# Kernel optimization log

Hardware: AMD Instinct MI355X
Metric: run time of the kernel (lower is better)

## Reference

```python
import jax, jax.numpy as jnp
import numpy as np

B, S, H = 2, 2048, 2048
NH, NKV, D = 32, 8, 64
N_REP = NH // NKV  # 4
THETA = 10000.0


def _rotate_half(x):
    x1, x2 = jnp.split(x, 2, axis=-1)
    return jnp.concatenate([-x2, x1], axis=-1)


def _apply_rope(q, k, position_ids):
    # q: [B,NH,S,D], k: [B,NKV,S,D], position_ids: [B,S]
    inv_freq = 1.0 / (THETA ** (jnp.arange(0, D, 2, dtype=jnp.float32) / D))  # [D/2]
    ang = position_ids[:, None, :, None].astype(jnp.float32) * inv_freq      # [B,1,S,D/2]
    cos = jnp.concatenate([jnp.cos(ang), jnp.cos(ang)], axis=-1)             # [B,1,S,D]
    sin = jnp.concatenate([jnp.sin(ang), jnp.sin(ang)], axis=-1)
    q = q * cos + _rotate_half(q) * sin
    k = k * cos + _rotate_half(k) * sin
    return q, k


def setup_inputs() -> dict:
    key = jax.random.key(0)
    k1, k2, k3, k4 = jax.random.split(key, 4)
    hidden_states = jax.random.normal(k1, (B, S, H), dtype=jnp.float32)
    position_ids = jnp.broadcast_to(jnp.arange(S, dtype=jnp.int64 if jax.config.jax_enable_x64 else jnp.int32)[None, :], (B, S))
    Wq = jax.random.normal(k2, (H, NH * D), dtype=jnp.float32) * 0.02
    Wkv = jax.random.normal(k3, (H, NKV * 2 * D), dtype=jnp.float32) * 0.02
    Wo = jax.random.normal(k4, (H, H), dtype=jnp.float32) * 0.02
    return {"hidden_states": hidden_states, "position_ids": position_ids,
            "Wq": Wq, "Wkv": Wkv, "Wo": Wo}


def reference(hidden_states, position_ids, Wq, Wkv, Wo):
    b, s, _ = hidden_states.shape
    # fused QKV projections (Linear, no bias)
    q = (hidden_states @ Wq).reshape(b, s, NH, D).transpose(0, 2, 1, 3)      # [B,NH,S,D]
    kv = (hidden_states @ Wkv).reshape(b, s, NKV, 2, D)
    k = kv[:, :, :, 0, :].transpose(0, 2, 1, 3)                              # [B,NKV,S,D]
    v = kv[:, :, :, 1, :].transpose(0, 2, 1, 3)                              # [B,NKV,S,D]
    # rotary embedding
    q, k = _apply_rope(q, k, position_ids)
    # GQA: repeat_interleave K/V heads
    k = jnp.repeat(k, N_REP, axis=1)                                         # [B,NH,S,D]
    v = jnp.repeat(v, N_REP, axis=1)
    # causal SDPA (eval mode: dropout_p = 0)
    scale = 1.0 / np.sqrt(D)
    scores = jnp.einsum('bhqd,bhkd->bhqk', q, k) * scale                     # [B,NH,S,S]
    causal = jnp.tril(jnp.ones((s, s), dtype=bool))
    scores = jnp.where(causal[None, None], scores, jnp.finfo(scores.dtype).min)
    probs = jax.nn.softmax(scores, axis=-1)
    ctx = jnp.einsum('bhqk,bhkd->bhqd', probs, v)                            # [B,NH,S,D]
    ctx = ctx.transpose(0, 2, 1, 3).reshape(b, s, H)
    return ctx @ Wo
```

## Files before the change

kernel.cpp:

```cpp
#include <hip/hip_runtime.h>

typedef __bf16 bf16_t;
typedef __bf16 bf16x8 __attribute__((ext_vector_type(8)));
typedef __bf16 bf16x4 __attribute__((ext_vector_type(4)));
typedef float f32x4 __attribute__((ext_vector_type(4)));

#define DEV static __device__ __forceinline__

DEV void gload16(const void* g, void* lds) {
  __builtin_amdgcn_global_load_lds((__attribute__((address_space(1))) void*)g,
                                   (__attribute__((address_space(3))) void*)lds, 16, 0, 0);
}

DEV f32x4 mfma16(bf16x8 a, bf16x8 b, f32x4 c) {
  return __builtin_amdgcn_mfma_f32_16x16x32_bf16(a, b, c, 0, 0, 0);
}

DEV void transpose_blk(const float* __restrict__ in, bf16_t* __restrict__ out,
                       int R, int C, int bx, int by, int tid, float (*tile)[33]) {
  const int tx = tid & 31, ty = tid >> 5;
  const int rb = by * 32, cb = bx * 32;
#pragma unroll
  for (int i = 0; i < 32; i += 8)
    tile[ty + i][tx] = in[(size_t)(rb + ty + i) * C + (cb + tx)];
  __syncthreads();
#pragma unroll
  for (int i = 0; i < 32; i += 8)
    out[(size_t)(cb + ty + i) * R + (rb + tx)] = (bf16_t)tile[tx][ty + i];
}

__global__ __launch_bounds__(256) void k_prep(const float* __restrict__ hs,
                                              bf16_t* __restrict__ Xbf,
                                              const float* __restrict__ Wq,
                                              const float* __restrict__ Wkv,
                                              const float* __restrict__ Wo,
                                              bf16_t* __restrict__ Wqkvt,
                                              bf16_t* __restrict__ Wot,
                                              const int* __restrict__ pos_ids,
                                              float2* __restrict__ tbl) {
  __shared__ float tile[32][33];
  const int bid = blockIdx.x, tid = threadIdx.x;
  if (bid < 8192) {
    const int i = (bid * 256 + tid) * 4;
    float4 v = *(const float4*)(hs + i);
    bf16x4 o;
    o[0] = (bf16_t)v.x; o[1] = (bf16_t)v.y; o[2] = (bf16_t)v.z; o[3] = (bf16_t)v.w;
    *(bf16x4*)(Xbf + i) = o;
  } else if (bid < 8192 + 512) {
    const int token = (bid - 8192) * 8 + (tid >> 5);
    const int d2 = tid & 31;
    const float p = (float)pos_ids[token];
    const float freq = exp2f(-(float)d2 / 32.0f * log2f(10000.0f));
    const float a = p * freq;
    tbl[token * 32 + d2] = make_float2(cosf(a), sinf(a));
  } else if (bid < 8192 + 512 + 4096) {
    const int local = bid - (8192 + 512);
    transpose_blk(Wq, Wqkvt, 2048, 2048, local & 63, local >> 6, tid, tile);
  } else if (bid < 8192 + 512 + 4096 + 2048) {
    const int local = bid - (8192 + 512 + 4096);
    transpose_blk(Wkv, Wqkvt + (size_t)2048 * 2048, 2048, 1024,
                  local & 31, local >> 5, tid, tile);
  } else {
    const int local = bid - (8192 + 512 + 4096 + 2048);
    transpose_blk(Wo, Wot, 2048, 2048, local & 63, local >> 6, tid, tile);
  }
}

#define PH_MID()                                            \
  __builtin_amdgcn_s_barrier();                             \
  asm volatile("s_waitcnt lgkmcnt(0)" ::: "memory");        \
  __builtin_amdgcn_sched_barrier(0);                        \
  __builtin_amdgcn_s_setprio(1)

#define PH_END()                                            \
  __builtin_amdgcn_s_setprio(0);                            \
  __builtin_amdgcn_s_barrier()

#define STAGE_A(bi, st, h)                                                      \
  do {                                                                          \
    const bf16_t* _s = gA + (size_t)(brow + (h) * 128 + r0) * gK + (st) * 64 + l0 * 8; \
    gload16(_s, &As[bi][((h) * 1024 + tid) * 8]);                               \
    gload16(_s + (size_t)64 * gK, &As[bi][((h) * 1024 + 512 + tid) * 8]);       \
  } while (0)

#define STAGE_B(bi, st, h)                                                      \
  do {                                                                          \
    const bf16_t* _s = gB + (size_t)(bcol + (h) * 128 + r0) * gK + (st) * 64 + l0 * 8; \
    gload16(_s, &Bs[bi][((h) * 1024 + tid) * 8]);                               \
    gload16(_s + (size_t)64 * gK, &Bs[bi][((h) * 1024 + 512 + tid) * 8]);       \
  } while (0)

#define LOADA(bi, mh)                                                           \
  _Pragma("unroll")                                                             \
  for (int mq = 0; mq < 4; ++mq) {                                              \
    const int R = wm * 128 + (mh) * 64 + mq * 16 + c15;                         \
    af[mq][0] = *(const bf16x8*)(&As[bi][(R * 8 + (g ^ (R & 7))) * 8]);         \
    af[mq][1] = *(const bf16x8*)(&As[bi][(R * 8 + ((4 + g) ^ (R & 7))) * 8]);   \
  }

#define LOADB(bi, nh)                                                           \
  _Pragma("unroll")                                                             \
  for (int nq = 0; nq < 2; ++nq) {                                              \
    const int R = wn * 64 + ((nh) * 2 + nq) * 16 + c15;                         \
    bfr[nq][0] = *(const bf16x8*)(&Bs[bi][(R * 8 + (g ^ (R & 7))) * 8]);        \
    bfr[nq][1] = *(const bf16x8*)(&Bs[bi][(R * 8 + ((4 + g) ^ (R & 7))) * 8]);  \
  }

#define MFMAQ(mh, nh)                                                           \
  _Pragma("unroll")                                                             \
  for (int nq = 0; nq < 2; ++nq)                                                \
    _Pragma("unroll")                                                           \
    for (int mq = 0; mq < 4; ++mq)                                              \
      acc[(mh) * 4 + mq][(nh) * 2 + nq] =                                       \
          mfma16(af[mq][1], bfr[nq][1],                                         \
                 mfma16(af[mq][0], bfr[nq][0], acc[(mh) * 4 + mq][(nh) * 2 + nq]));

__global__ __launch_bounds__(512, 2) void k_gemm_qkv(
    const bf16_t* __restrict__ gA, const bf16_t* __restrict__ gB,
    const float2* __restrict__ tbl,
    bf16_t* __restrict__ Qp, bf16_t* __restrict__ Kp, bf16_t* __restrict__ Vt) {
  __shared__ __align__(16) bf16_t As[2][256 * 64];
  __shared__ __align__(16) bf16_t Bs[2][256 * 64];
  const int gK = 2048, NBX = 12;
  const int tid = threadIdx.x;
  const int lane = tid & 63, w = tid >> 6;
  const int c15 = lane & 15, g = lane >> 4;
  const int wm = w >> 2, wn = w & 3;

  const int cpx = (int)gridDim.x >> 3;
  const int u = ((int)blockIdx.x & 7) * cpx + ((int)blockIdx.x >> 3);
  const int bx = u % NBX, by = u / NBX;
  const int brow = by * 256, bcol = bx * 256;

  const int r0 = tid >> 3, p0 = tid & 7;
  const int l0 = p0 ^ (r0 & 7);

  const f32x4 fzero = {0.f, 0.f, 0.f, 0.f};
  f32x4 acc[8][4];
#pragma unroll
  for (int m = 0; m < 8; ++m)
#pragma unroll
    for (int n = 0; n < 4; ++n) acc[m][n] = fzero;

  const int NT = gK >> 6;

  STAGE_A(0, 0, 0); STAGE_A(0, 0, 1); STAGE_B(0, 0, 0); STAGE_B(0, 0, 1);
  STAGE_A(1, 1, 0);
  asm volatile("s_waitcnt vmcnt(2)" ::: "memory");
  __builtin_amdgcn_s_barrier();

  for (int t = 0; t < NT; ++t) {
    const int bi = t & 1, oi = bi ^ 1;
    const int st1 = (t + 1 < NT) ? t + 1 : NT - 1;
    const int st2 = (t + 2 < NT) ? t + 2 : NT - 1;
    bf16x8 af[4][2], bfr[2][2];

    LOADA(bi, 0);
    LOADB(bi, 0);
    STAGE_A(oi, st1, 1);
    STAGE_B(oi, st1, 0);
    PH_MID();
    MFMAQ(0, 0);
    PH_END();

    LOADB(bi, 1);
    STAGE_B(oi, st1, 1);
    PH_MID();
    MFMAQ(0, 1);
    PH_END();

    LOADA(bi, 1);
    LOADB(bi, 0);
    PH_MID();
    MFMAQ(1, 0);
    PH_END();

    LOADB(bi, 1);
    STAGE_A(bi, st2, 0);
    asm volatile("s_waitcnt vmcnt(2)" ::: "memory");
    PH_MID();
    MFMAQ(1, 1);
    PH_END();
  }

  const int seg = bcol + wn * 64;
  const int wrow = brow + wm * 128;
  const float QSCALE = 0.125f * 1.44269504088896340736f;
  if (seg < 2048) {
    const int hq = seg >> 6;
#pragma unroll
    for (int m = 0; m < 8; ++m)
#pragma unroll
      for (int r = 0; r < 4; ++r) {
        const int row = wrow + m * 16 + g * 4 + r;
        const int bb = row >> 11, s = row & 2047;
        const float2 cs0 = tbl[row * 32 + c15];
        const float2 cs1 = tbl[row * 32 + 16 + c15];
        bf16_t* dst = Qp + (((size_t)bb * 32 + hq) * 2048 + s) * 64;
        dst[c15]      = (bf16_t)((acc[m][0][r] * cs0.x - acc[m][2][r] * cs0.y) * QSCALE);
        dst[32 + c15] = (bf16_t)((acc[m][2][r] * cs0.x + acc[m][0][r] * cs0.y) * QSCALE);
        dst[16 + c15] = (bf16_t)((acc[m][1][r] * cs1.x - acc[m][3][r] * cs1.y) * QSCALE);
        dst[48 + c15] = (bf16_t)((acc[m][3][r] * cs1.x + acc[m][1][r] * cs1.y) * QSCALE);
      }
  } else {
    const int cc = seg - 2048;
    const int kvh = cc >> 7;
    if (((cc >> 6) & 1) == 0) {
#pragma unroll
      for (int m = 0; m < 8; ++m)
#pragma unroll
        for (int r = 0; r < 4; ++r) {
          const int row = wrow + m * 16 + g * 4 + r;
          const int bb = row >> 11, s = row & 2047;
          const float2 cs0 = tbl[row * 32 + c15];
          const float2 cs1 = tbl[row * 32 + 16 + c15];
          bf16_t* dst = Kp + (((size_t)bb * 8 + kvh) * 2048 + s) * 64;
          dst[c15]      = (bf16_t)(acc[m][0][r] * cs0.x - acc[m][2][r] * cs0.y);
          dst[32 + c15] = (bf16_t)(acc[m][2][r] * cs0.x + acc[m][0][r] * cs0.y);
          dst[16 + c15] = (bf16_t)(acc[m][1][r] * cs1.x - acc[m][3][r] * cs1.y);
          dst[48 + c15] = (bf16_t)(acc[m][3][r] * cs1.x + acc[m][1][r] * cs1.y);
        }
    } else {
#pragma unroll
      for (int m = 0; m < 8; ++m) {
        const int row0 = wrow + m * 16 + g * 4;
        const int bb = row0 >> 11, s0 = row0 & 2047;
#pragma unroll
        for (int n = 0; n < 4; ++n) {
          bf16x4 o;
#pragma unroll
          for (int r = 0; r < 4; ++r) o[r] = (bf16_t)acc[m][n][r];
          const int d = n * 16 + c15;
          *(bf16x4*)(Vt + ((size_t)(bb * 8 + kvh) * 64 + d) * 2048 + s0) = o;
        }
      }
    }
  }
}

#define OSTAGE_A(bi, st, h)                                                     \
  do {                                                                          \
    const bf16_t* _s = gA + (size_t)(brow + (h) * 128 + r0) * gK + (st) * 64 + l0 * 8; \
    gload16(_s, &As[bi][((h) * 1024 + tid) * 8]);                               \
    gload16(_s + (size_t)64 * gK, &As[bi][((h) * 1024 + 512 + tid) * 8]);       \
  } while (0)

#define OSTAGE_B(bi, st)                                                        \
  do {                                                                          \
    const bf16_t* _s = gB + (size_t)(bcol + r0) * gK + (st) * 64 + l0 * 8;      \
    gload16(_s, &Bs[bi][tid * 8]);                                              \
    gload16(_s + (size_t)64 * gK, &Bs[bi][(512 + tid) * 8]);                    \
  } while (0)

#define OLOADB(bi)                                                              \
  _Pragma("unroll")                                                             \
  for (int nq = 0; nq < 2; ++nq) {                                              \
    const int R = wn * 32 + nq * 16 + c15;                                      \
    bfr[nq][0] = *(const bf16x8*)(&Bs[bi][(R * 8 + (g ^ (R & 7))) * 8]);        \
    bfr[nq][1] = *(const bf16x8*)(&Bs[bi][(R * 8 + ((4 + g) ^ (R & 7))) * 8]);  \
  }

#define OMFMAQ(mh)                                                              \
  _Pragma("unroll")                                                             \
  for (int nq = 0; nq < 2; ++nq)                                                \
    _Pragma("unroll")                                                           \
    for (int mq = 0; mq < 4; ++mq)                                              \
      acc[(mh) * 4 + mq][nq] =                                                  \
          mfma16(af[mq][1], bfr[nq][1],                                         \
                 mfma16(af[mq][0], bfr[nq][0], acc[(mh) * 4 + mq][nq]));

__global__ __launch_bounds__(512, 2) void k_gemm_out(
    const bf16_t* __restrict__ gA, const bf16_t* __restrict__ gB,
    float* __restrict__ C) {
  __shared__ __align__(16) bf16_t As[2][256 * 64];
  __shared__ __align__(16) bf16_t Bs[2][128 * 64];
  const int gK = 2048, NBX = 16, ldc = 2048;
  const int tid = threadIdx.x;
  const int lane = tid & 63, w = tid >> 6;
  const int c15 = lane & 15, g = lane >> 4;
  const int wm = w >> 2, wn = w & 3;

  const int cpx = (int)gridDim.x >> 3;
  const int u = ((int)blockIdx.x & 7) * cpx + ((int)blockIdx.x >> 3);
  const int bx = u % NBX, by = u / NBX;
  const int brow = by * 256, bcol = bx * 128;

  const int r0 = tid >> 3, p0 = tid & 7;
  const int l0 = p0 ^ (r0 & 7);

  const f32x4 fzero = {0.f, 0.f, 0.f, 0.f};
  f32x4 acc[8][2];
#pragma unroll
  for (int m = 0; m < 8; ++m)
#pragma unroll
    for (int n = 0; n < 2; ++n) acc[m][n] = fzero;

  const int NT = gK >> 6;

  OSTAGE_A(0, 0, 0); OSTAGE_A(0, 0, 1); OSTAGE_B(0, 0);
  OSTAGE_A(1, 1, 0); OSTAGE_B(1, 1);
  asm volatile("s_waitcnt vmcnt(4)" ::: "memory");
  __builtin_amdgcn_s_barrier();

  for (int t = 0; t < NT; ++t) {
    const int bi = t & 1, oi = bi ^ 1;
    const int st1 = (t + 1 < NT) ? t + 1 : NT - 1;
    const int st2 = (t + 2 < NT) ? t + 2 : NT - 1;
    bf16x8 af[4][2], bfr[2][2];

    LOADA(bi, 0);
    OLOADB(bi);
    OSTAGE_A(oi, st1, 1);
    PH_MID();
    OMFMAQ(0);
    PH_END();

    LOADA(bi, 1);
    OSTAGE_A(bi, st2, 0);
    OSTAGE_B(bi, st2);
    asm volatile("s_waitcnt vmcnt(4)" ::: "memory");
    PH_MID();
    OMFMAQ(1);
    PH_END();
  }

#pragma unroll
  for (int m = 0; m < 8; ++m)
#pragma unroll
    for (int n = 0; n < 2; ++n)
#pragma unroll
      for (int r = 0; r < 4; ++r) {
        const int row = brow + wm * 128 + m * 16 + g * 4 + r;
        const int col = bcol + wn * 32 + n * 16 + c15;
        C[(size_t)row * ldc + col] = acc[m][n][r];
      }
}

__global__ __launch_bounds__(256, 3) void k_attn(const bf16_t* __restrict__ Qp,
                                                 const bf16_t* __restrict__ Kp,
                                                 const bf16_t* __restrict__ Vt,
                                                 bf16_t* __restrict__ ctx) {
  const int wgid = blockIdx.x;
  const int gidx = wgid & 15;
  const int j    = wgid >> 4;
  const int b = gidx >> 3, kvh = gidx & 7;
  const int qs = 63 - j;
  const int tid = threadIdx.x, lane = tid & 63, w = tid >> 6;
  const int h = kvh * 4 + w;
  const int c15 = lane & 15, g = lane >> 4;

  __shared__ __align__(16) bf16_t Ks[2][64 * 64];
  __shared__ __align__(16) bf16_t Vs[2][64 * 64];
  __shared__ __align__(16) bf16_t Pw[4][32 * 64];
  bf16_t* pw = &Pw[w][0];

  const int q0 = qs * 32;

  bf16x8 aq[2][2];
#pragma unroll
  for (int m = 0; m < 2; ++m) {
    const bf16_t* Qrow = Qp + (((size_t)b * 32 + h) * 2048 + q0 + m * 16 + c15) * 64;
    aq[m][0] = *(const bf16x8*)(Qrow + g * 8);
    aq[m][1] = *(const bf16x8*)(Qrow + 32 + g * 8);
  }
  asm volatile("s_waitcnt vmcnt(0)" ::: "memory");

  const bf16_t* Kb = Kp + ((size_t)b * 8 + kvh) * (size_t)(2048 * 64);
  const bf16_t* Vb = Vt + ((size_t)b * 8 + kvh) * (size_t)(64 * 2048);

  const int c0 = tid,      r0 = c0 >> 3, l0 = (c0 & 7) ^ (r0 & 7);
  const int c1 = tid + 256, r1 = c1 >> 3, l1 = (c1 & 7) ^ (r1 & 7);
  const int dst0 = (w * 64) * 8, dst1 = (w * 64 + 256) * 8;

  const f32x4 fzero = {0.f, 0.f, 0.f, 0.f};
  f32x4 acc[2][4];
  f32x4 lsum[2];
#pragma unroll
  for (int m = 0; m < 2; ++m) {
    lsum[m] = fzero;
#pragma unroll
    for (int n = 0; n < 4; ++n) acc[m][n] = fzero;
  }
  bf16x8 bones;
#pragma unroll
  for (int j2 = 0; j2 < 8; ++j2) bones[j2] = (bf16_t)1.0f;

  const int ntw = qs / 2 + 1;

  gload16(Kb + (size_t)r0 * 64 + l0 * 8, &Ks[0][dst0]);
  gload16(Kb + (size_t)r1 * 64 + l1 * 8, &Ks[0][dst1]);
  gload16(Vb + (size_t)r0 * 2048 + l0 * 8, &Vs[0][dst0]);
  gload16(Vb + (size_t)r1 * 2048 + l1 * 8, &Vs[0][dst1]);

  for (int t = 0; t < ntw; ++t) {
    const int kvbase = t * 64;
    const int tnb = (t + 1 < ntw ? t + 1 : t) * 64;
    const int nb = (t + 1) & 1, cb = t & 1;

    gload16(Kb + (size_t)(tnb + r0) * 64 + l0 * 8, &Ks[nb][dst0]);
    gload16(Kb + (size_t)(tnb + r1) * 64 + l1 * 8, &Ks[nb][dst1]);
    gload16(Vb + (size_t)r0 * 2048 + tnb + l0 * 8, &Vs[nb][dst0]);
    gload16(Vb + (size_t)r1 * 2048 + tnb + l1 * 8, &Vs[nb][dst1]);
    asm volatile("s_waitcnt vmcnt(4)" ::: "memory");
    __builtin_amdgcn_s_barrier();

    const bf16_t* Kc = &Ks[cb][0];
    f32x4 sv[2][4];
    __builtin_amdgcn_s_setprio(1);
#pragma unroll
    for (int n = 0; n < 4; ++n) {
      const int row = n * 16 + c15;
      const bf16x8 bk0 = *(const bf16x8*)(Kc + row * 64 + ((g ^ (row & 7)) << 3));
      const bf16x8 bk1 = *(const bf16x8*)(Kc + row * 64 + (((4 + g) ^ (row & 7)) << 3));
      sv[0][n] = mfma16(aq[0][1], bk1, mfma16(aq[0][0], bk0, fzero));
      sv[1][n] = mfma16(aq[1][1], bk1, mfma16(aq[1][0], bk0, fzero));
    }
    __builtin_amdgcn_s_setprio(0);

    if (kvbase + 63 > q0) {
#pragma unroll
      for (int n = 0; n < 4; ++n)
#pragma unroll
        for (int r = 0; r < 4; ++r) {
          const int col = kvbase + n * 16 + c15;
          if (col > q0 + g * 4 + r)      sv[0][n][r] = -1e30f;
          if (col > q0 + 16 + g * 4 + r) sv[1][n][r] = -1e30f;
        }
    }
#pragma unroll
    for (int n = 0; n < 4; ++n)
#pragma unroll
      for (int r = 0; r < 4; ++r) {
        const int col = n * 16 + c15;
        const int rp0 = g * 4 + r, rp1 = 16 + g * 4 + r;
        pw[rp0 * 64 + ((((col >> 3) ^ (rp0 & 7)) << 3) | (col & 7))] = (bf16_t)exp2f(sv[0][n][r]);
        pw[rp1 * 64 + ((((col >> 3) ^ (rp1 & 7)) << 3) | (col & 7))] = (bf16_t)exp2f(sv[1][n][r]);
      }
    asm volatile("s_waitcnt lgkmcnt(0)" ::: "memory");
    __builtin_amdgcn_sched_barrier(0);

    bf16x8 ap[2][2];
#pragma unroll
    for (int m = 0; m < 2; ++m) {
      const int q = m * 16 + c15;
      ap[m][0] = *(const bf16x8*)(pw + q * 64 + ((g ^ (q & 7)) << 3));
      ap[m][1] = *(const bf16x8*)(pw + q * 64 + (((4 + g) ^ (q & 7)) << 3));
    }
    const bf16_t* Vc = &Vs[cb][0];
    __builtin_amdgcn_s_setprio(1);
#pragma unroll
    for (int m = 0; m < 2; ++m)
      lsum[m] = mfma16(ap[m][1], bones, mfma16(ap[m][0], bones, lsum[m]));
#pragma unroll
    for (int n = 0; n < 4; ++n) {
      const int row = n * 16 + c15;
      const bf16x8 bv0 = *(const bf16x8*)(Vc + row * 64 + ((g ^ (row & 7)) << 3));
      const bf16x8 bv1 = *(const bf16x8*)(Vc + row * 64 + (((4 + g) ^ (row & 7)) << 3));
#pragma unroll
      for (int m = 0; m < 2; ++m)
        acc[m][n] = mfma16(ap[m][1], bv1, mfma16(ap[m][0], bv0, acc[m][n]));
    }
    __builtin_amdgcn_s_setprio(0);
    __builtin_amdgcn_s_barrier();
  }

#pragma unroll
  for (int m = 0; m < 2; ++m) {
    float inv[4];
#pragma unroll
    for (int r = 0; r < 4; ++r) inv[r] = 1.0f / lsum[m][r];
#pragma unroll
    for (int n = 0; n < 4; ++n)
#pragma unroll
      for (int r = 0; r < 4; ++r) {
        const int rowq = q0 + m * 16 + g * 4 + r;
        const int col = h * 64 + n * 16 + c15;
        ctx[((size_t)b * 2048 + rowq) * 2048 + col] = (bf16_t)(acc[m][n][r] * inv[r]);
      }
  }
}

extern "C" void kernel_launch(void* const* d_in, const int* in_sizes, int n_in,
                              void* d_out, int out_size, void* d_ws, size_t ws_size,
                              hipStream_t stream) {
  const float* hs  = (const float*)d_in[0];
  const int*   pos = (const int*)d_in[1];
  const float* Wq  = (const float*)d_in[2];
  const float* Wkv = (const float*)d_in[3];
  const float* Wo  = (const float*)d_in[4];
  float* out = (float*)d_out;
  (void)in_sizes; (void)n_in; (void)out_size; (void)ws_size;

  char* p = (char*)d_ws;
  bf16_t* Xbf   = (bf16_t*)p; p += (size_t)4096 * 2048 * 2;
  bf16_t* Wqkvt = (bf16_t*)p; p += (size_t)3072 * 2048 * 2;
  bf16_t* Wot   = (bf16_t*)p; p += (size_t)2048 * 2048 * 2;
  float2* tbl   = (float2*)p; p += (size_t)4096 * 32 * 8;
  bf16_t* Qp    = (bf16_t*)p; p += (size_t)2 * 32 * 2048 * 64 * 2;
  bf16_t* Kp    = (bf16_t*)p; p += (size_t)2 * 8 * 2048 * 64 * 2;
  bf16_t* Vt    = (bf16_t*)p; p += (size_t)2 * 8 * 64 * 2048 * 2;
  bf16_t* ctx   = (bf16_t*)p; p += (size_t)4096 * 2048 * 2;

  k_prep<<<18944, 256, 0, stream>>>(hs, Xbf, Wq, Wkv, Wo, Wqkvt, Wot, pos, tbl);
  k_gemm_qkv<<<192, 512, 0, stream>>>(Xbf, Wqkvt, tbl, Qp, Kp, Vt);
  k_attn<<<1024, 256, 0, stream>>>(Qp, Kp, Vt, ctx);
  k_gemm_out<<<256, 512, 0, stream>>>(ctx, Wot, out);
}
```

Baseline: 188.8 us.

## Reorder QKV GEMM quadrants to reuse B fragments and restage whole tiles

The QKV GEMM's inner loop now walks the four quadrants in a serpentine order (00, 01, 11, 10), so each A and B register fragment is loaded from LDS once instead of reloading B. All staging of tile t+2 moves to the last two phases into the buffer just consumed, and the prologue stages both buffers fully with a deeper vmcnt wait. The output GEMM gets separate A fragment registers per half, which lets LDS reads overlap MFMAs. In exchange, register pressure rises, and the global prefetch now sits later in each iteration, which could expose memory latency.

```diff
diff --git a/kernel.cpp b/kernel.cpp
--- a/kernel.cpp
+++ b/kernel.cpp
@@ -90,30 +90,30 @@
     gload16(_s + (size_t)64 * gK, &Bs[bi][((h) * 1024 + 512 + tid) * 8]);       \
   } while (0)
 
-#define LOADA(bi, mh)                                                           \
+#define QLOADA(dst, bi, mh)                                                     \
   _Pragma("unroll")                                                             \
   for (int mq = 0; mq < 4; ++mq) {                                              \
     const int R = wm * 128 + (mh) * 64 + mq * 16 + c15;                         \
-    af[mq][0] = *(const bf16x8*)(&As[bi][(R * 8 + (g ^ (R & 7))) * 8]);         \
-    af[mq][1] = *(const bf16x8*)(&As[bi][(R * 8 + ((4 + g) ^ (R & 7))) * 8]);   \
-  }
-
-#define LOADB(bi, nh)                                                           \
+    dst[mq][0] = *(const bf16x8*)(&As[bi][(R * 8 + (g ^ (R & 7))) * 8]);        \
+    dst[mq][1] = *(const bf16x8*)(&As[bi][(R * 8 + ((4 + g) ^ (R & 7))) * 8]);  \
+  }
+
+#define QLOADB(dst, bi, nh)                                                     \
   _Pragma("unroll")                                                             \
   for (int nq = 0; nq < 2; ++nq) {                                              \
     const int R = wn * 64 + ((nh) * 2 + nq) * 16 + c15;                         \
-    bfr[nq][0] = *(const bf16x8*)(&Bs[bi][(R * 8 + (g ^ (R & 7))) * 8]);        \
-    bfr[nq][1] = *(const bf16x8*)(&Bs[bi][(R * 8 + ((4 + g) ^ (R & 7))) * 8]);  \
-  }
-
-#define MFMAQ(mh, nh)                                                           \
+    dst[nq][0] = *(const bf16x8*)(&Bs[bi][(R * 8 + (g ^ (R & 7))) * 8]);        \
+    dst[nq][1] = *(const bf16x8*)(&Bs[bi][(R * 8 + ((4 + g) ^ (R & 7))) * 8]);  \
+  }
+
+#define QMFMA(afX, bfX, mh, nh)                                                 \
   _Pragma("unroll")                                                             \
   for (int nq = 0; nq < 2; ++nq)                                                \
     _Pragma("unroll")                                                           \
     for (int mq = 0; mq < 4; ++mq)                                              \
       acc[(mh) * 4 + mq][(nh) * 2 + nq] =                                       \
-          mfma16(af[mq][1], bfr[nq][1],                                         \
-                 mfma16(af[mq][0], bfr[nq][0], acc[(mh) * 4 + mq][(nh) * 2 + nq]));
+          mfma16(afX[mq][1], bfX[nq][1],                                        \
+                 mfma16(afX[mq][0], bfX[nq][0], acc[(mh) * 4 + mq][(nh) * 2 + nq]));
 
 __global__ __launch_bounds__(512, 2) void k_gemm_qkv(
     const bf16_t* __restrict__ gA, const bf16_t* __restrict__ gB,
@@ -145,41 +145,38 @@
   const int NT = gK >> 6;
 
   STAGE_A(0, 0, 0); STAGE_A(0, 0, 1); STAGE_B(0, 0, 0); STAGE_B(0, 0, 1);
-  STAGE_A(1, 1, 0);
-  asm volatile("s_waitcnt vmcnt(2)" ::: "memory");
+  STAGE_A(1, 1, 0); STAGE_A(1, 1, 1); STAGE_B(1, 1, 0); STAGE_B(1, 1, 1);
+  asm volatile("s_waitcnt vmcnt(8)" ::: "memory");
   __builtin_amdgcn_s_barrier();
 
   for (int t = 0; t < NT; ++t) {
-    const int bi = t & 1, oi = bi ^ 1;
-    const int st1 = (t + 1 < NT) ? t + 1 : NT - 1;
+    const int bi = t & 1;
     const int st2 = (t + 2 < NT) ? t + 2 : NT - 1;
-    bf16x8 af[4][2], bfr[2][2];
-
-    LOADA(bi, 0);
-    LOADB(bi, 0);
-    STAGE_A(oi, st1, 1);
-    STAGE_B(oi, st1, 0);
+    bf16x8 af0[4][2], af1[4][2], bf0[2][2], bf1[2][2];
+
+    QLOADA(af0, bi, 0);
+    QLOADB(bf0, bi, 0);
     PH_MID();
-    MFMAQ(0, 0);
+    QMFMA(af0, bf0, 0, 0);
     PH_END();
 
-    LOADB(bi, 1);
-    STAGE_B(oi, st1, 1);
+    QLOADB(bf1, bi, 1);
     PH_MID();
-    MFMAQ(0, 1);
+    QMFMA(af0, bf1, 0, 1);
     PH_END();
 
-    LOADA(bi, 1);
-    LOADB(bi, 0);
+    QLOADA(af1, bi, 1);
+    STAGE_B(bi, st2, 0);
     PH_MID();
-    MFMAQ(1, 0);
+    QMFMA(af1, bf1, 1, 1);
     PH_END();
 
-    LOADB(bi, 1);
+    STAGE_B(bi, st2, 1);
     STAGE_A(bi, st2, 0);
-    asm volatile("s_waitcnt vmcnt(2)" ::: "memory");
+    STAGE_A(bi, st2, 1);
+    asm volatile("s_waitcnt vmcnt(8)" ::: "memory");
     PH_MID();
-    MFMAQ(1, 1);
+    QMFMA(af1, bf0, 1, 0);
     PH_END();
   }
 
@@ -252,6 +249,14 @@
     gload16(_s + (size_t)64 * gK, &Bs[bi][(512 + tid) * 8]);                    \
   } while (0)
 
+#define OLOADA(dst, bi, mh)                                                     \
+  _Pragma("unroll")                                                             \
+  for (int mq = 0; mq < 4; ++mq) {                                              \
+    const int R = wm * 128 + (mh) * 64 + mq * 16 + c15;                         \
+    dst[mq][0] = *(const bf16x8*)(&As[bi][(R * 8 + (g ^ (R & 7))) * 8]);        \
+    dst[mq][1] = *(const bf16x8*)(&As[bi][(R * 8 + ((4 + g) ^ (R & 7))) * 8]);  \
+  }
+
 #define OLOADB(bi)                                                              \
   _Pragma("unroll")                                                             \
   for (int nq = 0; nq < 2; ++nq) {                                              \
@@ -260,14 +265,14 @@
     bfr[nq][1] = *(const bf16x8*)(&Bs[bi][(R * 8 + ((4 + g) ^ (R & 7))) * 8]);  \
   }
 
-#define OMFMAQ(mh)                                                              \
+#define OMFMAQ(afX, mh)                                                         \
   _Pragma("unroll")                                                             \
   for (int nq = 0; nq < 2; ++nq)                                                \
     _Pragma("unroll")                                                           \
     for (int mq = 0; mq < 4; ++mq)                                              \
       acc[(mh) * 4 + mq][nq] =                                                  \
-          mfma16(af[mq][1], bfr[nq][1],                                         \
-                 mfma16(af[mq][0], bfr[nq][0], acc[(mh) * 4 + mq][nq]));
+          mfma16(afX[mq][1], bfr[nq][1],                                        \
+                 mfma16(afX[mq][0], bfr[nq][0], acc[(mh) * 4 + mq][nq]));
 
 __global__ __launch_bounds__(512, 2) void k_gemm_out(
     const bf16_t* __restrict__ gA, const bf16_t* __restrict__ gB,
@@ -306,21 +311,21 @@
     const int bi = t & 1, oi = bi ^ 1;
     const int st1 = (t + 1 < NT) ? t + 1 : NT - 1;
     const int st2 = (t + 2 < NT) ? t + 2 : NT - 1;
-    bf16x8 af[4][2], bfr[2][2];
-
-    LOADA(bi, 0);
+    bf16x8 af0[4][2], af1[4][2], bfr[2][2];
+
+    OLOADA(af0, bi, 0);
     OLOADB(bi);
     OSTAGE_A(oi, st1, 1);
     PH_MID();
-    OMFMAQ(0);
+    OMFMAQ(af0, 0);
     PH_END();
 
-    LOADA(bi, 1);
+    OLOADA(af1, bi, 1);
     OSTAGE_A(bi, st2, 0);
     OSTAGE_B(bi, st2);
     asm volatile("s_waitcnt vmcnt(4)" ::: "memory");
     PH_MID();
-    OMFMAQ(1);
+    OMFMAQ(af1, 1);
     PH_END();
   }
 
```

Result: no change. 190.0 us (+0.6%).
